# Performance work log

Hardware: AMD Instinct MI355X
Metric: run time of the kernel (lower is better)

Reference implementation:

```python
import jax, jax.numpy as jnp
import numpy as np

S, B, H, E = 2048, 4, 1024, 8
FF = 4 * H


def openai_gelu(x):
    # Megatron's tanh-approx gelu: 0.5*x*(1+tanh(sqrt(2/pi)*x*(1+0.044715*x^2)))
    return 0.5 * x * (1.0 + jnp.tanh(0.7978845608028654 * x * (1.0 + 0.044715 * x * x)))


def setup_inputs() -> dict:
    key = jax.random.key(0)
    ks = jax.random.split(key, 6)
    hidden_states = jax.random.normal(ks[0], (S, B, H), dtype=jnp.float32)
    # router: nn.Linear(H, E) with bias -> weight [E, H], bias [E]
    router_w = jax.random.normal(ks[1], (E, H), dtype=jnp.float32) / np.sqrt(H)
    router_b = jnp.zeros((E,), dtype=jnp.float32)
    # per-expert MLP weights, stacked on leading expert axis (torch Linear weight = [out, in])
    w1 = jax.random.normal(ks[2], (E, FF, H), dtype=jnp.float32) * np.sqrt(2.0 / (H + FF))
    b1 = jnp.zeros((E, FF), dtype=jnp.float32)
    w2 = jax.random.normal(ks[3], (E, H, FF), dtype=jnp.float32) * np.sqrt(2.0 / (H + FF))
    b2 = jnp.zeros((E, H), dtype=jnp.float32)
    return {"hidden_states": hidden_states, "router_w": router_w, "router_b": router_b,
            "w1": w1, "b1": b1, "w2": w2, "b2": b2}


def reference(hidden_states, router_w, router_b, w1, b1, w2, b2):
    s, b, h = hidden_states.shape
    e = w1.shape[0]
    # router + top-1 selection
    route = jax.nn.softmax(hidden_states @ router_w.T + router_b, axis=2)  # [s,b,E]
    max_prob = jnp.max(route, axis=2).reshape(-1, 1)                       # [N,1]
    max_ind = jnp.argmax(route, axis=2).reshape(-1)                        # [N]
    x = hidden_states.reshape(-1, h)                                       # [N,h]
    out = jnp.zeros_like(x)
    out_bias = jnp.zeros_like(x)
    # E is small and fixed; top-1 routing covers every token exactly once.
    for ei in range(e):
        inter = openai_gelu(x @ w1[ei].T + b1[ei])   # [N, 4h]
        y = inter @ w2[ei].T                          # [N, h]
        mask = (max_ind == ei)[:, None]
        out = jnp.where(mask, y, out)
        out_bias = jnp.where(mask, b2[ei][None, :], out_bias)
    out = (out * max_prob).reshape(s, b, h)
    out_bias = (out_bias * max_prob).reshape(s, b, h)
    return (out, out_bias)
```

## Files before the change

kernel.cpp:

```cpp
#include <hip/hip_runtime.h>
#include <math.h>

typedef float  f32x4  __attribute__((ext_vector_type(4)));
typedef short  bf16x8 __attribute__((ext_vector_type(8)));

#define NTOK 8192
#define H    1024
#define FF   4096
#define NEXP 8
#define MAXT128 72

__device__ __forceinline__ unsigned short f2bf(float f) {
    unsigned int u = __float_as_uint(f);
    u += 0x7fffu + ((u >> 16) & 1u);
    return (unsigned short)(u >> 16);
}

__device__ __forceinline__ void gload16(const void* g, void* l) {
    __builtin_amdgcn_global_load_lds((const __attribute__((address_space(1))) void*)g,
                                     (__attribute__((address_space(3))) void*)l, 16, 0, 0);
}

__global__ void __launch_bounds__(256)
router_k(const float* __restrict__ x, const float* __restrict__ rw, const float* __restrict__ rb,
         float* __restrict__ maxp, int* __restrict__ maxi, int* __restrict__ counts) {
    const int lane = threadIdx.x & 63;
    const int t = blockIdx.x * 4 + (threadIdx.x >> 6);
    const float4* xr = (const float4*)(x + (size_t)t * H);
    float acc[NEXP];
#pragma unroll
    for (int e = 0; e < NEXP; ++e) acc[e] = 0.f;
#pragma unroll
    for (int c = 0; c < 4; ++c) {
        float4 xv = xr[lane + 64 * c];
#pragma unroll
        for (int e = 0; e < NEXP; ++e) {
            float4 wv = ((const float4*)(rw + e * H))[lane + 64 * c];
            acc[e] += xv.x * wv.x + xv.y * wv.y + xv.z * wv.z + xv.w * wv.w;
        }
    }
#pragma unroll
    for (int e = 0; e < NEXP; ++e) {
#pragma unroll
        for (int off = 32; off > 0; off >>= 1) acc[e] += __shfl_xor(acc[e], off);
    }
    if (lane == 0) {
        float best = -1e30f; int bi = 0;
#pragma unroll
        for (int e = 0; e < NEXP; ++e) {
            float v = acc[e] + rb[e];
            acc[e] = v;
            if (v > best) { best = v; bi = e; }
        }
        float s = 0.f;
#pragma unroll
        for (int e = 0; e < NEXP; ++e) s += __expf(acc[e] - best);
        maxp[t] = 1.0f / s;
        maxi[t] = bi;
        atomicAdd(&counts[bi * 32], 1);
    }
}

__global__ void scan_k(const int* __restrict__ counts, int* __restrict__ offs,
                       int* __restrict__ tile_e, int* __restrict__ tile_r0, int* __restrict__ ntiles) {
    int off = 0, ti = 0;
    for (int e = 0; e < NEXP; ++e) {
        offs[e] = off;
        int nt = (counts[e * 32] + 127) >> 7;
        for (int j = 0; j < nt; ++j) { tile_e[ti] = e; tile_r0[ti] = off + (j << 7); ++ti; }
        off += nt << 7;
    }
    offs[NEXP] = off;
    *ntiles = ti;
}

__global__ void __launch_bounds__(256)
gather_k(const float* __restrict__ x, const int* __restrict__ maxi, const int* __restrict__ offs,
         int* __restrict__ cursor, int* __restrict__ perm, unsigned short* __restrict__ ab) {
    const int lane = threadIdx.x & 63;
    const int t = blockIdx.x * 4 + (threadIdx.x >> 6);
    int pos = 0;
    if (lane == 0) {
        int e = maxi[t];
        pos = offs[e] + atomicAdd(&cursor[e * 32], 1);
        perm[pos] = t;
    }
    pos = __shfl(pos, 0);
    const float4* xr = (const float4*)(x + (size_t)t * H);
    ushort4* ar = (ushort4*)(ab + (size_t)pos * H);
#pragma unroll
    for (int c = 0; c < 4; ++c) {
        float4 v = xr[lane + 64 * c];
        ar[lane + 64 * c] = make_ushort4(f2bf(v.x), f2bf(v.y), f2bf(v.z), f2bf(v.w));
    }
}

__global__ void __launch_bounds__(256)
cvt_k(const float4* __restrict__ w1, const float4* __restrict__ w2,
      ushort4* __restrict__ d1, ushort4* __restrict__ d2, int n4) {
    const int stride = gridDim.x * blockDim.x;
    for (int i = blockIdx.x * blockDim.x + threadIdx.x; i < n4; i += stride) {
        float4 v = w1[i]; d1[i] = make_ushort4(f2bf(v.x), f2bf(v.y), f2bf(v.z), f2bf(v.w));
        float4 u = w2[i]; d2[i] = make_ushort4(f2bf(u.x), f2bf(u.y), f2bf(u.z), f2bf(u.w));
    }
}

template<int KB>
__device__ __forceinline__ void gemm_core(const char* Ag, const char* Bg,
                                          unsigned short* As, unsigned short* Bs,
                                          f32x4 (&acc)[4][4]) {
    const int tid  = threadIdx.x;
    const int lane = tid & 63;
    const int wv   = tid >> 6;
    const int wr   = wv >> 1, wc = wv & 1;

    int goff[4];
#pragma unroll
    for (int c = 0; c < 4; ++c) {
        int op = c * 4096 + wv * 1024 + lane * 16;
        int ol = op ^ (((op >> 7) & 7) << 4);
        goff[c] = (ol >> 7) * KB + (ol & 127);
    }
    const int rA  = (wr * 64 + (lane & 15)) * 128;
    const int rB  = (wc * 64 + (lane & 15)) * 128;
    const int xr  = (lane & 7) << 4;
    const int cb0 = (lane >> 4) << 4;

#pragma unroll 1
    for (int kt = 0; kt < KB / 128; ++kt) {
        const int kb = kt * 128;
#pragma unroll
        for (int c = 0; c < 4; ++c)
            gload16(Ag + goff[c] + kb, (char*)As + c * 4096 + wv * 1024);
#pragma unroll
        for (int c = 0; c < 4; ++c)
            gload16(Bg + goff[c] + kb, (char*)Bs + c * 4096 + wv * 1024);
        __syncthreads();
#pragma unroll
        for (int kk = 0; kk < 2; ++kk) {
            bf16x8 a[4], b[4];
            const int cb = kk * 64 + cb0;
#pragma unroll
            for (int m = 0; m < 4; ++m)
                a[m] = *(const bf16x8*)((const char*)As + ((rA + m * 2048 + cb) ^ xr));
#pragma unroll
            for (int n = 0; n < 4; ++n)
                b[n] = *(const bf16x8*)((const char*)Bs + ((rB + n * 2048 + cb) ^ xr));
#pragma unroll
            for (int m = 0; m < 4; ++m)
#pragma unroll
                for (int n = 0; n < 4; ++n)
                    asm volatile("v_mfma_f32_16x16x32_bf16 %0, %1, %2, %0"
                                 : "+v"(acc[m][n]) : "v"(a[m]), "v"(b[n]));
        }
        __syncthreads();
    }
}

__global__ void __launch_bounds__(256)
gemm1_k(const unsigned short* __restrict__ ab, const unsigned short* __restrict__ w1b,
        const float* __restrict__ b1, unsigned short* __restrict__ inter,
        const int* __restrict__ tile_e, const int* __restrict__ tile_r0,
        const int* __restrict__ ntiles) {
    if ((int)blockIdx.y >= *ntiles) return;
    __shared__ alignas(16) unsigned short As[128 * 64];
    __shared__ alignas(16) unsigned short Bs[128 * 64];
    const int e    = tile_e[blockIdx.y];
    const int row0 = tile_r0[blockIdx.y];
    const int f0   = blockIdx.x * 128;
    f32x4 acc[4][4];
#pragma unroll
    for (int m = 0; m < 4; ++m)
#pragma unroll
        for (int n = 0; n < 4; ++n)
#pragma unroll
            for (int j = 0; j < 4; ++j) acc[m][n][j] = 0.f;

    gemm_core<2 * H>((const char*)(ab + (size_t)row0 * H),
                     (const char*)(w1b + ((size_t)e * FF + f0) * H), As, Bs, acc);

    const int lane = threadIdx.x & 63;
    const int wv = threadIdx.x >> 6, wr = wv >> 1, wc = wv & 1;
    const int lr = (lane >> 4) << 2, lc = lane & 15;
#pragma unroll
    for (int n = 0; n < 4; ++n) {
        const int gcol = f0 + wc * 64 + n * 16 + lc;
        const float bias = b1[e * FF + gcol];
#pragma unroll
        for (int m = 0; m < 4; ++m) {
            const int gr0 = row0 + wr * 64 + m * 16 + lr;
#pragma unroll
            for (int r = 0; r < 4; ++r) {
                float v = acc[m][n][r] + bias;
                float ex = __expf(1.5957691216057308f * v * (1.0f + 0.044715f * v * v));
                float u  = v - v / (ex + 1.0f);
                inter[(size_t)(gr0 + r) * FF + gcol] = f2bf(u);
            }
        }
    }
}

__global__ void __launch_bounds__(256)
gemm2_k(const unsigned short* __restrict__ inter, const unsigned short* __restrict__ w2b,
        const float* __restrict__ b2, float* __restrict__ out, float* __restrict__ outb,
        const int* __restrict__ tile_e, const int* __restrict__ tile_r0, const int* __restrict__ ntiles,
        const int* __restrict__ counts, const int* __restrict__ offs,
        const int* __restrict__ perm, const float* __restrict__ maxp) {
    const int bid = blockIdx.x;
    const int xb = bid & 7, yb = bid >> 3;
    if (yb >= *ntiles) return;
    __shared__ alignas(16) unsigned short As[128 * 64];
    __shared__ alignas(16) unsigned short Bs[128 * 64];
    const int e    = tile_e[yb];
    const int row0 = tile_r0[yb];
    const int h0   = xb * 128;
    f32x4 acc[4][4];
#pragma unroll
    for (int m = 0; m < 4; ++m)
#pragma unroll
        for (int n = 0; n < 4; ++n)
#pragma unroll
            for (int j = 0; j < 4; ++j) acc[m][n][j] = 0.f;

    gemm_core<2 * FF>((const char*)(inter + (size_t)row0 * FF),
                      (const char*)(w2b + ((size_t)e * H + h0) * FF), As, Bs, acc);

    const int lane = threadIdx.x & 63;
    const int wv = threadIdx.x >> 6, wr = wv >> 1, wc = wv & 1;
    const int lr = (lane >> 4) << 2, lc = lane & 15;
    const int cnt = counts[e * 32], offe = offs[e];
#pragma unroll
    for (int m = 0; m < 4; ++m) {
#pragma unroll
        for (int r = 0; r < 4; ++r) {
            const int grow = row0 + wr * 64 + m * 16 + lr + r;
            if (grow - offe < cnt) {
                const int t = perm[grow];
                const float p = maxp[t];
#pragma unroll
                for (int n = 0; n < 4; ++n) {
                    const int col = h0 + wc * 64 + n * 16 + lc;
                    out [(size_t)t * H + col] = acc[m][n][r] * p;
                    outb[(size_t)t * H + col] = b2[e * H + col] * p;
                }
            }
        }
    }
}

extern "C" void kernel_launch(void* const* d_in, const int* in_sizes, int n_in,
                              void* d_out, int out_size, void* d_ws, size_t ws_size,
                              hipStream_t stream) {
    const float* x  = (const float*)d_in[0];
    const float* rw = (const float*)d_in[1];
    const float* rb = (const float*)d_in[2];
    const float* w1 = (const float*)d_in[3];
    const float* b1 = (const float*)d_in[4];
    const float* w2 = (const float*)d_in[5];
    const float* b2 = (const float*)d_in[6];
    float* out  = (float*)d_out;
    float* outb = out + (size_t)NTOK * H;

    char* ws = (char*)d_ws;
    unsigned short* W1B   = (unsigned short*)(ws);
    unsigned short* W2B   = (unsigned short*)(ws + 67108864);
    unsigned short* AB    = (unsigned short*)(ws + 134217728);
    unsigned short* INTER = (unsigned short*)(ws + 153092096);
    float* MAXP    = (float*)(ws + 228589568);
    int*   MAXI    = (int*)  (ws + 228622336);
    int*   PERM    = (int*)  (ws + 228655104);
    int*   COUNTS  = (int*)  (ws + 228691968);
    int*   CURSOR  = (int*)  (ws + 228692992);
    int*   OFFS    = (int*)  (ws + 228694016);
    int*   TILE_E  = (int*)  (ws + 228694080);
    int*   TILE_R0 = (int*)  (ws + 228694592);
    int*   NTILES  = (int*)  (ws + 228695104);

    (void)hipMemsetAsync(COUNTS, 0, 2048, stream);

    router_k<<<NTOK / 4, 256, 0, stream>>>(x, rw, rb, MAXP, MAXI, COUNTS);
    scan_k<<<1, 1, 0, stream>>>(COUNTS, OFFS, TILE_E, TILE_R0, NTILES);
    gather_k<<<NTOK / 4, 256, 0, stream>>>(x, MAXI, OFFS, CURSOR, PERM, AB);
    cvt_k<<<4096, 256, 0, stream>>>((const float4*)w1, (const float4*)w2,
                                    (ushort4*)W1B, (ushort4*)W2B, NEXP * FF * H / 4);
    gemm1_k<<<dim3(FF / 128, MAXT128), 256, 0, stream>>>(AB, W1B, b1, INTER,
                                                         TILE_E, TILE_R0, NTILES);
    gemm2_k<<<8 * MAXT128, 256, 0, stream>>>(INTER, W2B, b2, out, outb,
                                             TILE_E, TILE_R0, NTILES,
                                             COUNTS, OFFS, PERM, MAXP);
}
```

Measured before the change: 348.4 us.

## Fuse fp32-to-bf16 weight conversion into GEMM B-tile loads, drop cvt kernel

Removes the standalone weight conversion kernel, which read all fp32 expert weights and wrote bf16 copies. The GEMMs now load fp32 weight rows directly into registers, convert them with packed bf16 conversion instructions, and store them swizzled into shared memory. This cuts a full pass over the weights and the extra write and read of the bf16 copy. In exchange, weight tiles are reread in fp32 by every token tile, doubling B-operand bytes per tile, and the asynchronous direct-to-LDS loads become synchronous register round trips that may stall the MFMA loop.

```diff
diff --git a/kernel.cpp b/kernel.cpp
--- a/kernel.cpp
+++ b/kernel.cpp
@@ -14,6 +14,10 @@
     unsigned int u = __float_as_uint(f);
     u += 0x7fffu + ((u >> 16) & 1u);
     return (unsigned short)(u >> 16);
+}
+
+__device__ __forceinline__ ushort4 cvt4(float4 v) {
+    return make_ushort4(f2bf(v.x), f2bf(v.y), f2bf(v.z), f2bf(v.w));
 }
 
 __device__ __forceinline__ void gload16(const void* g, void* l) {
@@ -91,21 +95,11 @@
 #pragma unroll
     for (int c = 0; c < 4; ++c) {
         float4 v = xr[lane + 64 * c];
-        ar[lane + 64 * c] = make_ushort4(f2bf(v.x), f2bf(v.y), f2bf(v.z), f2bf(v.w));
-    }
-}
-
-__global__ void __launch_bounds__(256)
-cvt_k(const float4* __restrict__ w1, const float4* __restrict__ w2,
-      ushort4* __restrict__ d1, ushort4* __restrict__ d2, int n4) {
-    const int stride = gridDim.x * blockDim.x;
-    for (int i = blockIdx.x * blockDim.x + threadIdx.x; i < n4; i += stride) {
-        float4 v = w1[i]; d1[i] = make_ushort4(f2bf(v.x), f2bf(v.y), f2bf(v.z), f2bf(v.w));
-        float4 u = w2[i]; d2[i] = make_ushort4(f2bf(u.x), f2bf(u.y), f2bf(u.z), f2bf(u.w));
-    }
-}
-
-template<int KB>
+        ar[lane + 64 * c] = cvt4(v);
+    }
+}
+
+template<int KB, int KBB>
 __device__ __forceinline__ void gemm_core(const char* Ag, const char* Bg,
                                           unsigned short* As, unsigned short* Bs,
                                           f32x4 (&acc)[4][4]) {
@@ -121,6 +115,16 @@
         int ol = op ^ (((op >> 7) & 7) << 4);
         goff[c] = (ol >> 7) * KB + (ol & 127);
     }
+    const int br  = tid >> 1;
+    const int bch = tid & 1;
+    const char* bsrc = Bg + (size_t)br * KBB + bch * 128;
+    char* bdst[4];
+#pragma unroll
+    for (int q = 0; q < 4; ++q) {
+        const int lcb = bch * 64 + q * 16;
+        bdst[q] = (char*)Bs + br * 128 + (lcb ^ ((br & 7) << 4));
+    }
+
     const int rA  = (wr * 64 + (lane & 15)) * 128;
     const int rB  = (wc * 64 + (lane & 15)) * 128;
     const int xr  = (lane & 7) << 4;
@@ -132,9 +136,19 @@
 #pragma unroll
         for (int c = 0; c < 4; ++c)
             gload16(Ag + goff[c] + kb, (char*)As + c * 4096 + wv * 1024);
-#pragma unroll
-        for (int c = 0; c < 4; ++c)
-            gload16(Bg + goff[c] + kb, (char*)Bs + c * 4096 + wv * 1024);
+        f32x4 t[8];
+#pragma unroll
+        for (int j = 0; j < 8; ++j)
+            t[j] = *(const f32x4*)(bsrc + kt * 256 + j * 16);
+#pragma unroll
+        for (int q = 0; q < 4; ++q) {
+            unsigned int o0, o1, o2, o3;
+            asm("v_cvt_pk_bf16_f32 %0, %1, %2" : "=v"(o0) : "v"(t[2*q][0]),   "v"(t[2*q][1]));
+            asm("v_cvt_pk_bf16_f32 %0, %1, %2" : "=v"(o1) : "v"(t[2*q][2]),   "v"(t[2*q][3]));
+            asm("v_cvt_pk_bf16_f32 %0, %1, %2" : "=v"(o2) : "v"(t[2*q+1][0]), "v"(t[2*q+1][1]));
+            asm("v_cvt_pk_bf16_f32 %0, %1, %2" : "=v"(o3) : "v"(t[2*q+1][2]), "v"(t[2*q+1][3]));
+            *(uint4*)bdst[q] = make_uint4(o0, o1, o2, o3);
+        }
         __syncthreads();
 #pragma unroll
         for (int kk = 0; kk < 2; ++kk) {
@@ -158,7 +172,7 @@
 }
 
 __global__ void __launch_bounds__(256)
-gemm1_k(const unsigned short* __restrict__ ab, const unsigned short* __restrict__ w1b,
+gemm1_k(const unsigned short* __restrict__ ab, const float* __restrict__ w1,
         const float* __restrict__ b1, unsigned short* __restrict__ inter,
         const int* __restrict__ tile_e, const int* __restrict__ tile_r0,
         const int* __restrict__ ntiles) {
@@ -176,8 +190,8 @@
 #pragma unroll
             for (int j = 0; j < 4; ++j) acc[m][n][j] = 0.f;
 
-    gemm_core<2 * H>((const char*)(ab + (size_t)row0 * H),
-                     (const char*)(w1b + ((size_t)e * FF + f0) * H), As, Bs, acc);
+    gemm_core<2 * H, 4 * H>((const char*)(ab + (size_t)row0 * H),
+                            (const char*)(w1 + ((size_t)e * FF + f0) * H), As, Bs, acc);
 
     const int lane = threadIdx.x & 63;
     const int wv = threadIdx.x >> 6, wr = wv >> 1, wc = wv & 1;
@@ -201,7 +215,7 @@
 }
 
 __global__ void __launch_bounds__(256)
-gemm2_k(const unsigned short* __restrict__ inter, const unsigned short* __restrict__ w2b,
+gemm2_k(const unsigned short* __restrict__ inter, const float* __restrict__ w2,
         const float* __restrict__ b2, float* __restrict__ out, float* __restrict__ outb,
         const int* __restrict__ tile_e, const int* __restrict__ tile_r0, const int* __restrict__ ntiles,
         const int* __restrict__ counts, const int* __restrict__ offs,
@@ -222,8 +236,8 @@
 #pragma unroll
             for (int j = 0; j < 4; ++j) acc[m][n][j] = 0.f;
 
-    gemm_core<2 * FF>((const char*)(inter + (size_t)row0 * FF),
-                      (const char*)(w2b + ((size_t)e * H + h0) * FF), As, Bs, acc);
+    gemm_core<2 * FF, 4 * FF>((const char*)(inter + (size_t)row0 * FF),
+                              (const char*)(w2 + ((size_t)e * H + h0) * FF), As, Bs, acc);
 
     const int lane = threadIdx.x & 63;
     const int wv = threadIdx.x >> 6, wr = wv >> 1, wc = wv & 1;
@@ -262,8 +276,6 @@
     float* outb = out + (size_t)NTOK * H;
 
     char* ws = (char*)d_ws;
-    unsigned short* W1B   = (unsigned short*)(ws);
-    unsigned short* W2B   = (unsigned short*)(ws + 67108864);
     unsigned short* AB    = (unsigned short*)(ws + 134217728);
     unsigned short* INTER = (unsigned short*)(ws + 153092096);
     float* MAXP    = (float*)(ws + 228589568);
@@ -281,11 +293,9 @@
     router_k<<<NTOK / 4, 256, 0, stream>>>(x, rw, rb, MAXP, MAXI, COUNTS);
     scan_k<<<1, 1, 0, stream>>>(COUNTS, OFFS, TILE_E, TILE_R0, NTILES);
     gather_k<<<NTOK / 4, 256, 0, stream>>>(x, MAXI, OFFS, CURSOR, PERM, AB);
-    cvt_k<<<4096, 256, 0, stream>>>((const float4*)w1, (const float4*)w2,
-                                    (ushort4*)W1B, (ushort4*)W2B, NEXP * FF * H / 4);
-    gemm1_k<<<dim3(FF / 128, MAXT128), 256, 0, stream>>>(AB, W1B, b1, INTER,
+    gemm1_k<<<dim3(FF / 128, MAXT128), 256, 0, stream>>>(AB, w1, b1, INTER,
                                                          TILE_E, TILE_R0, NTILES);
-    gemm2_k<<<8 * MAXT128, 256, 0, stream>>>(INTER, W2B, b2, out, outb,
+    gemm2_k<<<8 * MAXT128, 256, 0, stream>>>(INTER, w2, b2, out, outb,
                                              TILE_E, TILE_R0, NTILES,
                                              COUNTS, OFFS, PERM, MAXP);
 }
```

Measured after the change: 496.5 us. 1.43x slower.
